# Kernel tuning notes

Hardware: AMD Instinct MI355X
Metric: run time of the kernel (lower is better)

Reference implementation:

```python
import jax, jax.numpy as jnp
import numpy as np

B, N, DIM_IN, DIM_OUT, EMBED, DP = 8, 1024, 64, 64, 16, 16


def setup_inputs() -> dict:
    key = jax.random.key(0)
    k1, k2, k3, k4, k5 = jax.random.split(key, 5)
    x = jax.random.normal(k1, (B, N, DIM_IN), dtype=jnp.float32)
    node_embed = jax.random.normal(k2, (N, EMBED), dtype=jnp.float32)
    prompt_answer = jax.random.normal(k3, (B, N, DP), dtype=jnp.float32)
    # kaiming-normal-like init for the pools (gain irrelevant for correctness testing)
    weights_pool = jax.random.normal(k4, (EMBED, 2, DIM_IN, DIM_OUT), dtype=jnp.float32) * (2.0 / (2 * DIM_IN * DIM_OUT)) ** 0.5
    bias_pool = jax.random.normal(k5, (EMBED, DIM_OUT), dtype=jnp.float32) * (2.0 / DIM_OUT) ** 0.5
    return {"x": x, "node_embed": node_embed, "prompt_answer": prompt_answer,
            "weights_pool": weights_pool, "bias_pool": bias_pool}


def reference(x, node_embed, prompt_answer, weights_pool, bias_pool):
    n = node_embed.shape[0]
    # adaptive adjacency: softmax(relu(E E^T)) over rows' last dim (torch dim=1 on 2D)
    sim = jax.nn.softmax(jax.nn.relu(node_embed @ node_embed.T), axis=1)  # [N,N]
    supports = jnp.stack([jnp.eye(n, dtype=x.dtype), sim], axis=0)        # [2,N,N]
    # node-adaptive weights/bias
    weights = jnp.einsum('nd,dkio->nkio', node_embed, weights_pool)       # [N,2,I,O]
    bias = node_embed @ bias_pool                                         # [N,O]
    # sub-support from L1 cdist; torch softmax dim=1 of [B,N,N] -> axis=1
    d1 = jnp.sum(jnp.abs(prompt_answer[:, :, None, :] - prompt_answer[:, None, :, :]), axis=-1)  # [B,N,N]
    sub = jax.nn.softmax(-jax.nn.relu(d1), axis=1)                        # [B,N,N]
    # supports' = supports @ sub (sub expanded over k=2); then x_g = supports' @ x.
    # Associate as supports @ (sub @ x) to avoid the [B,2,N,N] intermediate.
    sx = jnp.einsum('bmc,bcd->bmd', sub, x)                               # [B,N,I]  (sub @ x)
    x_g = jnp.einsum('knm,bmc->bknc', supports, sx)                       # [B,2,N,I]
    x_g = jnp.transpose(x_g, (0, 2, 1, 3))                                # [B,N,2,I]
    return jnp.einsum('bnki,nkio->bno', x_g, weights) + bias              # [B,N,O]
```

## Files before the change

kernel.cpp:

```cpp
#include <hip/hip_runtime.h>

#define BB 8
#define NN 1024
#define DIN 64
#define DOUT 64
#define EMB 16
#define DPC 16

typedef __attribute__((ext_vector_type(8))) short bf16x8;
typedef __attribute__((ext_vector_type(4))) float f32x4;

__device__ inline unsigned short f2bf(float f) {
    unsigned u = __float_as_uint(f);
    u += 0x7fffu + ((u >> 16) & 1u);
    return (unsigned short)(u >> 16);
}

__global__ __launch_bounds__(256) void k_front(const float* __restrict__ E,
                                               const float* __restrict__ pa,
                                               const float* __restrict__ x,
                                               const float* __restrict__ wp,
                                               unsigned short* __restrict__ sim_bf,
                                               unsigned short* __restrict__ Sub,
                                               unsigned short* __restrict__ xzT,
                                               unsigned short* __restrict__ W2) {
    __shared__ __align__(16) char smem[36096];
    const int bid = blockIdx.x;
    const int tid = threadIdx.x;

    if (bid < 256) {
        const int b = bid >> 5, c0 = (bid & 31) * 32;
        float* pa_l  = (float*)smem;
        float* myp   = (float*)(smem + 32768);
        float* zpart = (float*)(smem + 34816);
        float* invZ  = (float*)(smem + 35840);

        if (tid < 128)
            ((float4*)myp)[tid] = *(const float4*)&pa[((size_t)b*NN + c0)*DPC + tid*4];
        __syncthreads();

        const int cs = tid & 31, jq = tid >> 5;
        float myc[DPC];
        #pragma unroll
        for (int p4 = 0; p4 < 4; ++p4) {
            float4 t = *(const float4*)&myp[cs*DPC + p4*4];
            myc[p4*4+0] = t.x; myc[p4*4+1] = t.y; myc[p4*4+2] = t.z; myc[p4*4+3] = t.w;
        }

        float part = 0.0f;
        for (int h = 0; h < 2; ++h) {
            __syncthreads();
            for (int i = tid; i < 512*DPC/4; i += 256)
                ((float4*)pa_l)[i] = ((const float4*)(pa + ((size_t)b*NN + h*512)*DPC))[i];
            __syncthreads();
            unsigned short* subrow = Sub + ((size_t)b*NN + (c0 + cs))*NN + h*512 + jq*64;
            for (int j4 = 0; j4 < 16; ++j4) {
                float e[4];
                #pragma unroll
                for (int t = 0; t < 4; ++t) {
                    int jj = jq*64 + j4*4 + t;
                    float s = 0.0f;
                    #pragma unroll
                    for (int p4 = 0; p4 < 4; ++p4) {
                        float4 q = *(const float4*)&pa_l[jj*DPC + p4*4];
                        s += fabsf(myc[p4*4+0]-q.x) + fabsf(myc[p4*4+1]-q.y)
                           + fabsf(myc[p4*4+2]-q.z) + fabsf(myc[p4*4+3]-q.w);
                    }
                    e[t] = __expf(-s);
                }
                part += e[0] + e[1] + e[2] + e[3];
                *(ushort4*)&subrow[j4*4] =
                    make_ushort4(f2bf(e[0]), f2bf(e[1]), f2bf(e[2]), f2bf(e[3]));
            }
        }
        zpart[jq*32 + cs] = part;
        __syncthreads();
        float* xl = pa_l;
        #pragma unroll
        for (int i = 0; i < 8; ++i) {
            int l = i*256 + tid, d = l & 63, c = l >> 6;
            xl[c*65 + d] = x[((size_t)b*NN + c0 + c)*DIN + d];
        }
        if (tid < 32) {
            float z = 0.f;
            #pragma unroll
            for (int q = 0; q < 8; ++q) z += zpart[q*32 + tid];
            invZ[tid] = 1.0f / z;
        }
        __syncthreads();
        #pragma unroll
        for (int i = 0; i < 8; ++i) {
            int l = i*256 + tid, c = l & 31, d = l >> 5;
            xzT[((size_t)b*DIN + d)*NN + c0 + c] = f2bf(xl[c*65 + d] * invZ[c]);
        }
    } else if (bid < 512) {
        const int idx = bid - 256;
        const int kio0 = (idx & 7) * 1024 + tid * 4;
        const int n0 = (idx >> 3) * 32;
        float* El = (float*)smem;
        if (tid < 128) *(float4*)&El[tid*4] = *(const float4*)&E[n0*EMB + tid*4];

        float4 wq[EMB];
        #pragma unroll
        for (int d = 0; d < EMB; ++d)
            wq[d] = *(const float4*)&wp[d*8192 + kio0];
        __syncthreads();

        for (int n = 0; n < 32; ++n) {
            float4 a = make_float4(0.f, 0.f, 0.f, 0.f);
            #pragma unroll
            for (int d = 0; d < EMB; ++d) {
                float e = El[n*EMB + d];
                a.x += e*wq[d].x; a.y += e*wq[d].y; a.z += e*wq[d].z; a.w += e*wq[d].w;
            }
            *(ushort4*)&W2[(size_t)(n0 + n)*8192 + kio0] =
                make_ushort4(f2bf(a.x), f2bf(a.y), f2bf(a.z), f2bf(a.w));
        }
    } else {
        const int i = bid - 512;
        const int lane = tid & 63, wave = tid >> 6;
        float* redw = (float*)smem;

        float4 ei0 = *(const float4*)&E[i*EMB + 0];
        float4 ei1 = *(const float4*)&E[i*EMB + 4];
        float4 ei2 = *(const float4*)&E[i*EMB + 8];
        float4 ei3 = *(const float4*)&E[i*EMB + 12];

        float rv[4], tmax = -1e30f;
        #pragma unroll
        for (int k = 0; k < 4; ++k) {
            int j = tid + k*256;
            float4 a0 = *(const float4*)&E[j*EMB + 0];
            float4 a1 = *(const float4*)&E[j*EMB + 4];
            float4 a2 = *(const float4*)&E[j*EMB + 8];
            float4 a3 = *(const float4*)&E[j*EMB + 12];
            float s = ei0.x*a0.x + ei0.y*a0.y + ei0.z*a0.z + ei0.w*a0.w
                    + ei1.x*a1.x + ei1.y*a1.y + ei1.z*a1.z + ei1.w*a1.w
                    + ei2.x*a2.x + ei2.y*a2.y + ei2.z*a2.z + ei2.w*a2.w
                    + ei3.x*a3.x + ei3.y*a3.y + ei3.z*a3.z + ei3.w*a3.w;
            s = fmaxf(s, 0.0f);
            rv[k] = s; tmax = fmaxf(tmax, s);
        }
        #pragma unroll
        for (int off = 32; off > 0; off >>= 1) tmax = fmaxf(tmax, __shfl_xor(tmax, off));
        if (lane == 0) redw[wave] = tmax;
        __syncthreads();
        float rmax = fmaxf(fmaxf(redw[0], redw[1]), fmaxf(redw[2], redw[3]));
        __syncthreads();

        float ev[4], tsum = 0.f;
        #pragma unroll
        for (int k = 0; k < 4; ++k) { ev[k] = __expf(rv[k] - rmax); tsum += ev[k]; }
        #pragma unroll
        for (int off = 32; off > 0; off >>= 1) tsum += __shfl_xor(tsum, off);
        if (lane == 0) redw[wave] = tsum;
        __syncthreads();
        float inv = 1.0f / (redw[0] + redw[1] + redw[2] + redw[3]);
        #pragma unroll
        for (int k = 0; k < 4; ++k)
            sim_bf[(size_t)i*NN + tid + k*256] = f2bf(ev[k] * inv);
    }
}

#define ASTR 72
#define BSTR 72

__device__ inline void gemm_tile(const unsigned short* __restrict__ Arow,
                                 const unsigned short* __restrict__ Brow,
                                 unsigned short* A_l, unsigned short* B_l,
                                 int tid, f32x4& acc) {
    const int lane = tid & 63, wave = tid >> 6;
    const int q = lane >> 4, r = lane & 15;

    const int brow_ = tid >> 2, bch = (tid & 3) * 2;
    const int arow_ = tid >> 3, ach = tid & 7;

    uint4 pb0 = *(const uint4*)&Brow[(size_t)brow_*NN + (bch+0)*8];
    uint4 pb1 = *(const uint4*)&Brow[(size_t)brow_*NN + (bch+1)*8];
    uint4 pa0;
    if (tid < 128) pa0 = *(const uint4*)&Arow[(size_t)arow_*NN + ach*8];

    for (int kk = 0; kk < 16; ++kk) {
        __syncthreads();
        *(uint4*)&B_l[brow_*BSTR + (bch+0)*8] = pb0;
        *(uint4*)&B_l[brow_*BSTR + (bch+1)*8] = pb1;
        if (tid < 128) *(uint4*)&A_l[arow_*ASTR + ach*8] = pa0;
        __syncthreads();
        if (kk < 15) {
            int c1 = (kk + 1) * 64;
            pb0 = *(const uint4*)&Brow[(size_t)brow_*NN + c1 + (bch+0)*8];
            pb1 = *(const uint4*)&Brow[(size_t)brow_*NN + c1 + (bch+1)*8];
            if (tid < 128) pa0 = *(const uint4*)&Arow[(size_t)arow_*NN + c1 + ach*8];
        }
        bf16x8 a0 = *(const bf16x8*)&A_l[r*ASTR + q*8];
        bf16x8 b0 = *(const bf16x8*)&B_l[(wave*16 + r)*BSTR + q*8];
        acc = __builtin_amdgcn_mfma_f32_16x16x32_bf16(a0, b0, acc, 0, 0, 0);
        bf16x8 a1 = *(const bf16x8*)&A_l[r*ASTR + 32 + q*8];
        bf16x8 b1 = *(const bf16x8*)&B_l[(wave*16 + r)*BSTR + 32 + q*8];
        acc = __builtin_amdgcn_mfma_f32_16x16x32_bf16(a1, b1, acc, 0, 0, 0);
    }
}

__global__ __launch_bounds__(256) void k_sx4(const unsigned short* __restrict__ Sub,
                                             const unsigned short* __restrict__ xzT,
                                             float* __restrict__ sx,
                                             unsigned short* __restrict__ sxT) {
    const int b = blockIdx.y, m0 = blockIdx.x * 16;
    const int tid = threadIdx.x, lane = tid & 63, wave = tid >> 6;
    __shared__ __align__(16) unsigned short A_l[16 * ASTR];
    __shared__ __align__(16) unsigned short B_l[64 * BSTR];

    f32x4 acc = {0.f, 0.f, 0.f, 0.f};
    gemm_tile(Sub + ((size_t)b*NN + m0)*NN, xzT + (size_t)b*DIN*NN, A_l, B_l, tid, acc);

    const int q = lane >> 4, r = lane & 15;
    const int d = wave*16 + r;
    const int mrow = m0 + q*4;
    #pragma unroll
    for (int reg = 0; reg < 4; ++reg)
        sx[((size_t)b*NN + mrow + reg)*DIN + d] = acc[reg];
    *(ushort4*)&sxT[((size_t)b*DIN + d)*NN + mrow] =
        make_ushort4(f2bf(acc[0]), f2bf(acc[1]), f2bf(acc[2]), f2bf(acc[3]));
}

__global__ __launch_bounds__(256) void k_y4(const unsigned short* __restrict__ sim_bf,
                                            const unsigned short* __restrict__ sxT,
                                            float* __restrict__ y) {
    const int b = blockIdx.y, m0 = blockIdx.x * 16;
    const int tid = threadIdx.x, lane = tid & 63, wave = tid >> 6;
    __shared__ __align__(16) unsigned short A_l[16 * ASTR];
    __shared__ __align__(16) unsigned short B_l[64 * BSTR];

    f32x4 acc = {0.f, 0.f, 0.f, 0.f};
    gemm_tile(sim_bf + (size_t)m0*NN, sxT + (size_t)b*DIN*NN, A_l, B_l, tid, acc);

    const int q = lane >> 4, r = lane & 15;
    const int d = wave*16 + r;
    const int mrow = m0 + q*4;
    #pragma unroll
    for (int reg = 0; reg < 4; ++reg)
        y[((size_t)b*NN + mrow + reg)*DIN + d] = acc[reg];
}

__global__ __launch_bounds__(256) void k_out2(const float* __restrict__ E,
                                              const float* __restrict__ bp,
                                              const unsigned short* __restrict__ W2,
                                              const float* __restrict__ sxin,
                                              const float* __restrict__ yin,
                                              float* __restrict__ out) {
    const int n = blockIdx.x;
    const int tid = threadIdx.x;
    __shared__ __align__(16) uint4 W2l4[1024];
    __shared__ float vl[BB * 128];
    __shared__ float El2[EMB];

    if (tid < EMB) El2[tid] = E[n*EMB + tid];
    {
        const uint4* src = (const uint4*)(W2 + (size_t)n * 8192);
        #pragma unroll
        for (int r = 0; r < 4; ++r) W2l4[tid + r*256] = src[tid + r*256];
    }
    for (int idx = tid; idx < BB*128; idx += 256) {
        int b_ = idx >> 7, ki = idx & 127;
        vl[idx] = (ki < 64) ? sxin[((size_t)b_*NN + n)*DIN + ki]
                            : yin[((size_t)b_*NN + n)*DIN + (ki - 64)];
    }
    __syncthreads();

    const int b_ = tid >> 5, op = (tid & 31) * 2;
    const unsigned* W2u = (const unsigned*)W2l4;
    float a0 = 0.f, a1 = 0.f;
    #pragma unroll 4
    for (int ki = 0; ki < 128; ++ki) {
        float vv = vl[b_*128 + ki];
        unsigned w2 = W2u[ki*32 + (op >> 1)];
        a0 += vv * __uint_as_float(w2 << 16);
        a1 += vv * __uint_as_float(w2 & 0xffff0000u);
    }
    float b0 = 0.f, b1 = 0.f;
    #pragma unroll
    for (int d = 0; d < EMB; ++d) {
        float e = El2[d];
        b0 += e * bp[d*DOUT + op];
        b1 += e * bp[d*DOUT + op + 1];
    }
    *(float2*)&out[((size_t)b_*NN + n)*DOUT + op] = make_float2(a0 + b0, a1 + b1);
}

extern "C" void kernel_launch(void* const* d_in, const int* in_sizes, int n_in,
                              void* d_out, int out_size, void* d_ws, size_t ws_size,
                              hipStream_t stream) {
    (void)in_sizes; (void)n_in; (void)out_size; (void)ws_size;
    const float* x  = (const float*)d_in[0];
    const float* E  = (const float*)d_in[1];
    const float* pa = (const float*)d_in[2];
    const float* wp = (const float*)d_in[3];
    const float* bp = (const float*)d_in[4];
    float* out = (float*)d_out;

    unsigned short* ws16   = (unsigned short*)d_ws;
    unsigned short* sim_bf = ws16;
    unsigned short* xzT    = sim_bf + (size_t)NN*NN;
    unsigned short* sxT    = xzT + (size_t)BB*DIN*NN;
    unsigned short* Sub    = sxT + (size_t)BB*DIN*NN;
    unsigned short* W2     = Sub + (size_t)BB*NN*NN;
    float* sx = (float*)(W2 + (size_t)NN*2*DIN*DOUT);
    float* y  = sx + (size_t)BB*NN*DIN;

    k_front<<<1536, 256, 0, stream>>>(E, pa, x, wp, sim_bf, Sub, xzT, W2);
    k_sx4<<<dim3(64, BB), 256, 0, stream>>>(Sub, xzT, sx, sxT);
    k_y4<<<dim3(64, BB), 256, 0, stream>>>(sim_bf, sxT, y);
    k_out2<<<NN, 256, 0, stream>>>(E, bp, W2, sx, y, out);
}
```

Baseline: 118.9 us.

## Fuse output projection into y GEMM using MFMA over transposed weight pool

Stops materialising the per-node weight tensor W2 (N×2×64×64 bf16). Instead the output is computed as x_g · weights_pool with MFMA per embedding dim, then contracted with each node's embedding, and this runs inside the y GEMM kernel, which removes the separate k_out2 launch and the fp32 sx/y round trips. k_front now only transposes the weight pool to bf16, and sx is stored as bf16. The fused kernel does 16x more MFMA work per tile and reads the full WPT from global per block, and storing sx in bf16 lowers precision.

```diff
diff --git a/kernel.cpp b/kernel.cpp
--- a/kernel.cpp
+++ b/kernel.cpp
@@ -23,7 +23,7 @@
                                                unsigned short* __restrict__ sim_bf,
                                                unsigned short* __restrict__ Sub,
                                                unsigned short* __restrict__ xzT,
-                                               unsigned short* __restrict__ W2) {
+                                               unsigned short* __restrict__ WPT) {
     __shared__ __align__(16) char smem[36096];
     const int bid = blockIdx.x;
     const int tid = threadIdx.x;
@@ -93,31 +93,8 @@
             int l = i*256 + tid, c = l & 31, d = l >> 5;
             xzT[((size_t)b*DIN + d)*NN + c0 + c] = f2bf(xl[c*65 + d] * invZ[c]);
         }
-    } else if (bid < 512) {
-        const int idx = bid - 256;
-        const int kio0 = (idx & 7) * 1024 + tid * 4;
-        const int n0 = (idx >> 3) * 32;
-        float* El = (float*)smem;
-        if (tid < 128) *(float4*)&El[tid*4] = *(const float4*)&E[n0*EMB + tid*4];
-
-        float4 wq[EMB];
-        #pragma unroll
-        for (int d = 0; d < EMB; ++d)
-            wq[d] = *(const float4*)&wp[d*8192 + kio0];
-        __syncthreads();
-
-        for (int n = 0; n < 32; ++n) {
-            float4 a = make_float4(0.f, 0.f, 0.f, 0.f);
-            #pragma unroll
-            for (int d = 0; d < EMB; ++d) {
-                float e = El[n*EMB + d];
-                a.x += e*wq[d].x; a.y += e*wq[d].y; a.z += e*wq[d].z; a.w += e*wq[d].w;
-            }
-            *(ushort4*)&W2[(size_t)(n0 + n)*8192 + kio0] =
-                make_ushort4(f2bf(a.x), f2bf(a.y), f2bf(a.z), f2bf(a.w));
-        }
-    } else {
-        const int i = bid - 512;
+    } else if (bid < 1280) {
+        const int i = bid - 256;
         const int lane = tid & 63, wave = tid >> 6;
         float* redw = (float*)smem;
 
@@ -159,6 +136,26 @@
         #pragma unroll
         for (int k = 0; k < 4; ++k)
             sim_bf[(size_t)i*NN + tid + k*256] = f2bf(ev[k] * inv);
+    } else {
+        const int d = bid - 1280;
+        float* wpl = (float*)smem;
+        const float* wsrc = wp + (size_t)d * 8192;
+        for (int i = tid; i < 2048; i += 256)
+            ((float4*)wpl)[i] = ((const float4*)wsrc)[i];
+        __syncthreads();
+        const int o = tid & 63, g = tid >> 6;
+        #pragma unroll
+        for (int k = 0; k < 2; ++k) {
+            unsigned short tmp[16];
+            #pragma unroll
+            for (int t = 0; t < 16; ++t)
+                tmp[t] = f2bf(wpl[k*4096 + (g*16 + t)*64 + o]);
+            unsigned short* dst = WPT + (size_t)(d*64 + o)*128 + k*64 + g*16;
+            #pragma unroll
+            for (int t4 = 0; t4 < 4; ++t4)
+                *(ushort4*)&dst[t4*4] =
+                    make_ushort4(tmp[t4*4], tmp[t4*4+1], tmp[t4*4+2], tmp[t4*4+3]);
+        }
     }
 }
 
@@ -203,7 +200,7 @@
 
 __global__ __launch_bounds__(256) void k_sx4(const unsigned short* __restrict__ Sub,
                                              const unsigned short* __restrict__ xzT,
-                                             float* __restrict__ sx,
+                                             unsigned short* __restrict__ sx_bf,
                                              unsigned short* __restrict__ sxT) {
     const int b = blockIdx.y, m0 = blockIdx.x * 16;
     const int tid = threadIdx.x, lane = tid & 63, wave = tid >> 6;
@@ -216,75 +213,105 @@
     const int q = lane >> 4, r = lane & 15;
     const int d = wave*16 + r;
     const int mrow = m0 + q*4;
-    #pragma unroll
-    for (int reg = 0; reg < 4; ++reg)
-        sx[((size_t)b*NN + mrow + reg)*DIN + d] = acc[reg];
-    *(ushort4*)&sxT[((size_t)b*DIN + d)*NN + mrow] =
-        make_ushort4(f2bf(acc[0]), f2bf(acc[1]), f2bf(acc[2]), f2bf(acc[3]));
-}
-
-__global__ __launch_bounds__(256) void k_y4(const unsigned short* __restrict__ sim_bf,
-                                            const unsigned short* __restrict__ sxT,
-                                            float* __restrict__ y) {
+    unsigned short h0 = f2bf(acc[0]), h1 = f2bf(acc[1]), h2 = f2bf(acc[2]), h3 = f2bf(acc[3]);
+    sx_bf[((size_t)b*NN + mrow + 0)*DIN + d] = h0;
+    sx_bf[((size_t)b*NN + mrow + 1)*DIN + d] = h1;
+    sx_bf[((size_t)b*NN + mrow + 2)*DIN + d] = h2;
+    sx_bf[((size_t)b*NN + mrow + 3)*DIN + d] = h3;
+    *(ushort4*)&sxT[((size_t)b*DIN + d)*NN + mrow] = make_ushort4(h0, h1, h2, h3);
+}
+
+#define S2 136
+#define PSTR 65
+
+__global__ __launch_bounds__(256) void k_y_out(const unsigned short* __restrict__ sim_bf,
+                                               const unsigned short* __restrict__ sxT,
+                                               const unsigned short* __restrict__ sx_bf,
+                                               const unsigned short* __restrict__ WPT,
+                                               const float* __restrict__ E,
+                                               const float* __restrict__ bp,
+                                               float* __restrict__ out) {
     const int b = blockIdx.y, m0 = blockIdx.x * 16;
     const int tid = threadIdx.x, lane = tid & 63, wave = tid >> 6;
     __shared__ __align__(16) unsigned short A_l[16 * ASTR];
     __shared__ __align__(16) unsigned short B_l[64 * BSTR];
+    __shared__ __align__(16) unsigned short A2[16 * S2];
+    __shared__ float E16[16 * EMB];
+    __shared__ float bpl[EMB * DOUT];
+    __shared__ float part[4 * 16 * PSTR];
+
+    E16[tid] = E[(size_t)m0 * EMB + tid];
+    ((float4*)bpl)[tid] = ((const float4*)bp)[tid];
+    if (tid < 128) {
+        int row = tid >> 3, c8 = (tid & 7) * 8;
+        *(uint4*)&A2[row*S2 + c8] =
+            *(const uint4*)&sx_bf[((size_t)b*NN + m0 + row)*DIN + c8];
+    }
 
     f32x4 acc = {0.f, 0.f, 0.f, 0.f};
     gemm_tile(sim_bf + (size_t)m0*NN, sxT + (size_t)b*DIN*NN, A_l, B_l, tid, acc);
 
     const int q = lane >> 4, r = lane & 15;
-    const int d = wave*16 + r;
-    const int mrow = m0 + q*4;
     #pragma unroll
     for (int reg = 0; reg < 4; ++reg)
-        y[((size_t)b*NN + mrow + reg)*DIN + d] = acc[reg];
-}
-
-__global__ __launch_bounds__(256) void k_out2(const float* __restrict__ E,
-                                              const float* __restrict__ bp,
-                                              const unsigned short* __restrict__ W2,
-                                              const float* __restrict__ sxin,
-                                              const float* __restrict__ yin,
-                                              float* __restrict__ out) {
-    const int n = blockIdx.x;
-    const int tid = threadIdx.x;
-    __shared__ __align__(16) uint4 W2l4[1024];
-    __shared__ float vl[BB * 128];
-    __shared__ float El2[EMB];
-
-    if (tid < EMB) El2[tid] = E[n*EMB + tid];
+        A2[(q*4 + reg)*S2 + 64 + wave*16 + r] = f2bf(acc[reg]);
+    __syncthreads();
+
+    bf16x8 af[4];
+    #pragma unroll
+    for (int ks = 0; ks < 4; ++ks)
+        af[ks] = *(const bf16x8*)&A2[r*S2 + ks*32 + q*8];
+
+    f32x4 pacc[16];
+    #pragma unroll
+    for (int i = 0; i < 16; ++i) pacc[i] = (f32x4){0.f, 0.f, 0.f, 0.f};
+
+    const unsigned short* wbase = WPT + ((size_t)(wave*256 + r))*128 + q*8;
+    #pragma unroll
+    for (int nfl = 0; nfl < 16; ++nfl) {
+        const unsigned short* bb = wbase + (size_t)nfl * 16 * 128;
+        #pragma unroll
+        for (int ks = 0; ks < 4; ++ks) {
+            bf16x8 bf_ = *(const bf16x8*)(bb + ks*32);
+            pacc[nfl] = __builtin_amdgcn_mfma_f32_16x16x32_bf16(af[ks], bf_, pacc[nfl], 0, 0, 0);
+        }
+    }
+
+    float po[4][4];
+    #pragma unroll
+    for (int reg = 0; reg < 4; ++reg)
+        #pragma unroll
+        for (int ohi = 0; ohi < 4; ++ohi) po[reg][ohi] = 0.f;
+    #pragma unroll
+    for (int nfl = 0; nfl < 16; ++nfl) {
+        const int dd = nfl >> 2, ohi = nfl & 3;
+        #pragma unroll
+        for (int reg = 0; reg < 4; ++reg)
+            po[reg][ohi] += E16[(q*4 + reg)*EMB + wave*4 + dd] * pacc[nfl][reg];
+    }
+    #pragma unroll
+    for (int reg = 0; reg < 4; ++reg)
+        #pragma unroll
+        for (int ohi = 0; ohi < 4; ++ohi)
+            part[wave*16*PSTR + (q*4 + reg)*PSTR + ohi*16 + r] = po[reg][ohi];
+    __syncthreads();
+
     {
-        const uint4* src = (const uint4*)(W2 + (size_t)n * 8192);
-        #pragma unroll
-        for (int r = 0; r < 4; ++r) W2l4[tid + r*256] = src[tid + r*256];
-    }
-    for (int idx = tid; idx < BB*128; idx += 256) {
-        int b_ = idx >> 7, ki = idx & 127;
-        vl[idx] = (ki < 64) ? sxin[((size_t)b_*NN + n)*DIN + ki]
-                            : yin[((size_t)b_*NN + n)*DIN + (ki - 64)];
-    }
-    __syncthreads();
-
-    const int b_ = tid >> 5, op = (tid & 31) * 2;
-    const unsigned* W2u = (const unsigned*)W2l4;
-    float a0 = 0.f, a1 = 0.f;
-    #pragma unroll 4
-    for (int ki = 0; ki < 128; ++ki) {
-        float vv = vl[b_*128 + ki];
-        unsigned w2 = W2u[ki*32 + (op >> 1)];
-        a0 += vv * __uint_as_float(w2 << 16);
-        a1 += vv * __uint_as_float(w2 & 0xffff0000u);
-    }
-    float b0 = 0.f, b1 = 0.f;
-    #pragma unroll
-    for (int d = 0; d < EMB; ++d) {
-        float e = El2[d];
-        b0 += e * bp[d*DOUT + op];
-        b1 += e * bp[d*DOUT + op + 1];
-    }
-    *(float2*)&out[((size_t)b_*NN + n)*DOUT + op] = make_float2(a0 + b0, a1 + b1);
+        const int row = tid >> 4, o4 = (tid & 15) * 4;
+        float4 res;
+        #pragma unroll
+        for (int j = 0; j < 4; ++j) {
+            const int o = o4 + j;
+            float s = part[0*16*PSTR + row*PSTR + o] + part[1*16*PSTR + row*PSTR + o]
+                    + part[2*16*PSTR + row*PSTR + o] + part[3*16*PSTR + row*PSTR + o];
+            float bsum = 0.f;
+            #pragma unroll
+            for (int d = 0; d < EMB; ++d)
+                bsum += E16[row*EMB + d] * bpl[d*DOUT + o];
+            ((float*)&res)[j] = s + bsum;
+        }
+        *(float4*)&out[((size_t)b*NN + m0 + row)*DOUT + o4] = res;
+    }
 }
 
 extern "C" void kernel_launch(void* const* d_in, const int* in_sizes, int n_in,
@@ -303,12 +330,10 @@
     unsigned short* xzT    = sim_bf + (size_t)NN*NN;
     unsigned short* sxT    = xzT + (size_t)BB*DIN*NN;
     unsigned short* Sub    = sxT + (size_t)BB*DIN*NN;
-    unsigned short* W2     = Sub + (size_t)BB*NN*NN;
-    float* sx = (float*)(W2 + (size_t)NN*2*DIN*DOUT);
-    float* y  = sx + (size_t)BB*NN*DIN;
-
-    k_front<<<1536, 256, 0, stream>>>(E, pa, x, wp, sim_bf, Sub, xzT, W2);
-    k_sx4<<<dim3(64, BB), 256, 0, stream>>>(Sub, xzT, sx, sxT);
-    k_y4<<<dim3(64, BB), 256, 0, stream>>>(sim_bf, sxT, y);
-    k_out2<<<NN, 256, 0, stream>>>(E, bp, W2, sx, y, out);
-}
+    unsigned short* sx_bf  = Sub + (size_t)BB*NN*NN;
+    unsigned short* WPT    = sx_bf + (size_t)BB*NN*DIN;
+
+    k_front<<<1296, 256, 0, stream>>>(E, pa, x, wp, sim_bf, Sub, xzT, WPT);
+    k_sx4<<<dim3(64, BB), 256, 0, stream>>>(Sub, xzT, sx_bf, sxT);
+    k_y_out<<<dim3(64, BB), 256, 0, stream>>>(sim_bf, sxT, sx_bf, WPT, E, bp, out);
+}
```

Measured after the change: 120.4 us. Within noise of the previous version (+1.3%).
